# Kernel optimization log

Hardware: AMD Instinct MI355X
Metric: run time of the kernel (lower is better)

Reference implementation:

```python
import jax, jax.numpy as jnp
import numpy as np

B, FDIM = 8192, 2048
S = 10000          # number of sign nodes
D = 100            # num diseases
E = 500000         # number of 'finding' edges
ETA = 0.01


def setup_inputs() -> dict:
    key = jax.random.key(0)
    k1, k2, k3, k4, k5 = jax.random.split(key, 5)
    grad_output_batch = jax.random.normal(k1, (B, FDIM), dtype=jnp.float32)
    # similarity of each sign node per sample (0 => sign not found)
    sims = jax.random.uniform(k2, (B, S), dtype=jnp.float32)
    edge_weight = jax.random.uniform(k3, (E,), dtype=jnp.float32)
    edge_src = jax.random.randint(k4, (E,), 0, D)   # disease node per edge
    edge_dst = jax.random.randint(k5, (E,), 0, S)   # sign node per edge
    return {
        "grad_output_batch": grad_output_batch,
        "sims": sims,
        "edge_weight": edge_weight,
        "edge_src": edge_src,
        "edge_dst": edge_dst,
        "num_diseases": D,
    }


def reference(grad_output_batch, sims, edge_weight, edge_src, edge_dst, num_diseases):
    # Scatter-add edge weights into disease x sign matrix A[d, s]
    A = jnp.zeros((num_diseases, sims.shape[1]), dtype=sims.dtype)
    A = A.at[edge_src, edge_dst].add(edge_weight)
    # Per-sample gradient norm g_i = ||grad_output_batch[i]||_2
    g = jnp.linalg.norm(grad_output_batch, axis=1)            # [B]
    # nudges[i, d] = eta * g_i * sum_s sims[i, s] * A[d, s]
    nudges = ETA * g[:, None] * jnp.einsum('bs,ds->bd', sims, A)
    return nudges
```

## Files before the change

### kernel.cpp

```cpp
#include <hip/hip_runtime.h>
#include <hip/hip_bf16.h>

#define B_DIM   8192
#define FDIM    2048
#define S_DIM   10000
#define D_DIM   100
#define E_NUM   500000
#define ETA     0.01f

#define DPAD    112
#define NT      7
#define KSTEPS  313
#define KBLK    1252

typedef float  f32x4  __attribute__((ext_vector_type(4)));
typedef short  s16x8  __attribute__((ext_vector_type(8)));
typedef __bf16 bf16x8 __attribute__((ext_vector_type(8)));

__device__ inline unsigned short f2bf_bits(float x) {
    unsigned int u = __float_as_uint(x);
    unsigned int r = u + 0x7FFFu + ((u >> 16) & 1u);
    return (unsigned short)(r >> 16);
}

__global__ void scatter_kernel(const float* __restrict__ ew,
                               const int* __restrict__ esrc,
                               const int* __restrict__ edst,
                               float* __restrict__ A) {
    int e = blockIdx.x * 256 + threadIdx.x;
    if (e < E_NUM) {
        atomicAdd(&A[(size_t)esrc[e] * S_DIM + edst[e]], ew[e]);
    }
}

__global__ void build_asw_kernel(const float* __restrict__ A,
                                 unsigned short* __restrict__ Asw) {
    int t = blockIdx.x * 256 + threadIdx.x;
    int kb  = t / 896;
    int rem = t - kb * 896;
    int d   = rem >> 3;
    int s   = kb * 8 + (rem & 7);
    float v = (d < D_DIM && s < S_DIM) ? A[d * S_DIM + s] : 0.f;
    Asw[t] = f2bf_bits(v);
}

__global__ void norm_kernel(const float* __restrict__ go, float* __restrict__ g) {
    int wave = threadIdx.x >> 6;
    int lane = threadIdx.x & 63;
    int row  = blockIdx.x * 4 + wave;
    const f32x4* p = (const f32x4*)(go + (size_t)row * FDIM);
    float s = 0.f;
#pragma unroll
    for (int j = 0; j < 8; ++j) {
        f32x4 v = __builtin_nontemporal_load(p + lane + 64 * j);
        s += v[0]*v[0] + v[1]*v[1] + v[2]*v[2] + v[3]*v[3];
    }
#pragma unroll
    for (int off = 32; off; off >>= 1) s += __shfl_xor(s, off);
    if (lane == 0) g[row] = sqrtf(s);
}

__device__ inline s16x8 cvt_a(f32x4 f0, f32x4 f1) {
    bf16x8 abf;
    abf[0] = (__bf16)f0[0]; abf[1] = (__bf16)f0[1];
    abf[2] = (__bf16)f0[2]; abf[3] = (__bf16)f0[3];
    abf[4] = (__bf16)f1[0]; abf[5] = (__bf16)f1[1];
    abf[6] = (__bf16)f1[2]; abf[7] = (__bf16)f1[3];
    return __builtin_bit_cast(s16x8, abf);
}

__global__ __launch_bounds__(512, 4)
void gemm_kernel(const float* __restrict__ sims,
                 const unsigned short* __restrict__ Asw,
                 const float* __restrict__ g,
                 float* __restrict__ out) {
    __shared__ float red[8][64][29];
    const int tid  = threadIdx.x;
    const int wave = tid >> 6;
    const int lane = tid & 63;
    const int lhi  = lane >> 4;
    const int llo  = lane & 15;
    const int i0   = blockIdx.x * 16;

    const float* srow = sims + (size_t)(i0 + llo) * S_DIM + 8 * lhi;

    f32x4 acc[NT];
#pragma unroll
    for (int n = 0; n < NT; ++n) acc[n] = 0.f;

    int t = wave;
    f32x4 f0, f1;
    {
        const f32x4* p = (const f32x4*)(srow + t * 32);
        f0 = p[0]; f1 = p[1];
    }
    for (; t < 312; t += 8) {
        f32x4 n0, n1;
        n0 = 0.f; n1 = 0.f;
        const int tn = t + 8;
        if (tn < 312) {
            const f32x4* p = (const f32x4*)(srow + tn * 32);
            n0 = p[0]; n1 = p[1];
        }

        const unsigned short* bbase = Asw + ((size_t)(4 * t + lhi) * DPAD + llo) * 8;
        s16x8 b0 = *(const s16x8*)(bbase);
        s16x8 b1 = *(const s16x8*)(bbase + 128);
        s16x8 b2 = *(const s16x8*)(bbase + 256);
        s16x8 b3 = *(const s16x8*)(bbase + 384);
        s16x8 b4 = *(const s16x8*)(bbase + 512);
        s16x8 b5 = *(const s16x8*)(bbase + 640);
        s16x8 b6 = *(const s16x8*)(bbase + 768);

        s16x8 a = cvt_a(f0, f1);
        acc[0] = __builtin_amdgcn_mfma_f32_16x16x32_bf16(a, b0, acc[0], 0, 0, 0);
        acc[1] = __builtin_amdgcn_mfma_f32_16x16x32_bf16(a, b1, acc[1], 0, 0, 0);
        acc[2] = __builtin_amdgcn_mfma_f32_16x16x32_bf16(a, b2, acc[2], 0, 0, 0);
        acc[3] = __builtin_amdgcn_mfma_f32_16x16x32_bf16(a, b3, acc[3], 0, 0, 0);
        acc[4] = __builtin_amdgcn_mfma_f32_16x16x32_bf16(a, b4, acc[4], 0, 0, 0);
        acc[5] = __builtin_amdgcn_mfma_f32_16x16x32_bf16(a, b5, acc[5], 0, 0, 0);
        acc[6] = __builtin_amdgcn_mfma_f32_16x16x32_bf16(a, b6, acc[6], 0, 0, 0);

        f0 = n0; f1 = n1;
    }

    if (wave == 0) {
        f32x4 t0, t1;
        t0 = 0.f; t1 = 0.f;
        if (lhi < 2) {
            const f32x4* p = (const f32x4*)(srow + 312 * 32);
            t0 = p[0]; t1 = p[1];
        }
        const unsigned short* bbase = Asw + ((size_t)(4 * 312 + lhi) * DPAD + llo) * 8;
        s16x8 a = cvt_a(t0, t1);
#pragma unroll
        for (int n = 0; n < NT; ++n) {
            s16x8 b = *(const s16x8*)(bbase + n * 128);
            acc[n] = __builtin_amdgcn_mfma_f32_16x16x32_bf16(a, b, acc[n], 0, 0, 0);
        }
    }

#pragma unroll
    for (int n = 0; n < NT; ++n)
#pragma unroll
        for (int r = 0; r < 4; ++r)
            red[wave][lane][n * 4 + r] = acc[n][r];
    __syncthreads();

    if (wave == 0) {
        float gi[4];
#pragma unroll
        for (int r = 0; r < 4; ++r)
            gi[r] = ETA * g[i0 + lhi * 4 + r];
#pragma unroll
        for (int n = 0; n < NT; ++n) {
            int col = n * 16 + llo;
#pragma unroll
            for (int r = 0; r < 4; ++r) {
                float v = 0.f;
#pragma unroll
                for (int w = 0; w < 8; ++w) v += red[w][lane][n * 4 + r];
                if (col < D_DIM) {
                    int row = i0 + lhi * 4 + r;
                    out[row * D_DIM + col] = gi[r] * v;
                }
            }
        }
    }
}

extern "C" void kernel_launch(void* const* d_in, const int* in_sizes, int n_in,
                              void* d_out, int out_size, void* d_ws, size_t ws_size,
                              hipStream_t stream) {
    const float* grad = (const float*)d_in[0];
    const float* sims = (const float*)d_in[1];
    const float* ew   = (const float*)d_in[2];
    const int*   esrc = (const int*)d_in[3];
    const int*   edst = (const int*)d_in[4];
    float* out = (float*)d_out;

    char* ws = (char*)d_ws;
    float*          A   = (float*)ws;
    unsigned short* Asw = (unsigned short*)(ws + 4000000);
    float*          g   = (float*)(ws + 4000000 + 2243584);

    hipMemsetAsync(A, 0, (size_t)D_DIM * S_DIM * sizeof(float), stream);

    scatter_kernel  <<<(E_NUM + 255) / 256, 256, 0, stream>>>(ew, esrc, edst, A);
    build_asw_kernel<<<(KBLK * DPAD * 8) / 256, 256, 0, stream>>>(A, Asw);
    norm_kernel     <<<B_DIM / 4, 256, 0, stream>>>(grad, g);
    gemm_kernel     <<<B_DIM / 16, 512, 0, stream>>>(sims, Asw, g, out);
}
```

Measured before the change: 551.8 us.

## Restructure GEMM to split-K with LDS-shared B tiles and separate reduce

The GEMM is reorganized so each block covers 128 rows and one of 8 K-slices. Each B tile (Asw) is staged once per step into double-buffered LDS and shared by all 8 waves, instead of every wave loading B from global memory for its own K steps over 16 rows. Partial results go to a workspace slab per K-slice, and a new reduce kernel sums them and applies the eta*g scaling. This trades B-operand reuse for extra partial-sum traffic (8 slabs of B*D floats), an additional launch, and a __syncthreads each K step.

```diff
diff --git a/kernel.cpp b/kernel.cpp
--- a/kernel.cpp
+++ b/kernel.cpp
@@ -11,6 +11,8 @@
 #define DPAD    112
 #define NT      7
 #define KSTEPS  313
+#define KSPLIT  8
+#define MROWS   128
 #define KBLK    1252
 
 typedef float  f32x4  __attribute__((ext_vector_type(4)));
@@ -72,45 +74,64 @@
 __global__ __launch_bounds__(512, 4)
 void gemm_kernel(const float* __restrict__ sims,
                  const unsigned short* __restrict__ Asw,
-                 const float* __restrict__ g,
-                 float* __restrict__ out) {
-    __shared__ float red[8][64][29];
+                 float* __restrict__ part) {
+    __shared__ unsigned short buf[2][3584];
     const int tid  = threadIdx.x;
     const int wave = tid >> 6;
     const int lane = tid & 63;
     const int lhi  = lane >> 4;
     const int llo  = lane & 15;
-    const int i0   = blockIdx.x * 16;
 
-    const float* srow = sims + (size_t)(i0 + llo) * S_DIM + 8 * lhi;
+    const int kb = blockIdx.x & 7;
+    const int rb = blockIdx.x >> 3;
+    const int t0 = (KSTEPS * kb) >> 3;
+    const int t1 = (KSTEPS * (kb + 1)) >> 3;
+    const int nsteps = t1 - t0;
+
+    const int row0 = rb * MROWS + wave * 16;
+    const float* srow = sims + (size_t)(row0 + llo) * S_DIM + 8 * lhi;
 
     f32x4 acc[NT];
 #pragma unroll
     for (int n = 0; n < NT; ++n) acc[n] = 0.f;
 
-    int t = wave;
+    if (tid < 448) {
+        s16x8 v = *(const s16x8*)(Asw + (size_t)t0 * 3584 + tid * 8);
+        *(s16x8*)&buf[0][tid * 8] = v;
+    }
     f32x4 f0, f1;
     {
-        const f32x4* p = (const f32x4*)(srow + t * 32);
+        const f32x4* p = (const f32x4*)(srow + t0 * 32);
         f0 = p[0]; f1 = p[1];
     }
-    for (; t < 312; t += 8) {
-        f32x4 n0, n1;
-        n0 = 0.f; n1 = 0.f;
-        const int tn = t + 8;
-        if (tn < 312) {
-            const f32x4* p = (const f32x4*)(srow + tn * 32);
-            n0 = p[0]; n1 = p[1];
+    __syncthreads();
+
+    for (int i = 0; i < nsteps; ++i) {
+        const int t = t0 + i;
+        const int cur = i & 1;
+
+        if (i + 1 < nsteps && tid < 448) {
+            s16x8 v = *(const s16x8*)(Asw + (size_t)(t + 1) * 3584 + tid * 8);
+            *(s16x8*)&buf[cur ^ 1][tid * 8] = v;
         }
 
-        const unsigned short* bbase = Asw + ((size_t)(4 * t + lhi) * DPAD + llo) * 8;
-        s16x8 b0 = *(const s16x8*)(bbase);
-        s16x8 b1 = *(const s16x8*)(bbase + 128);
-        s16x8 b2 = *(const s16x8*)(bbase + 256);
-        s16x8 b3 = *(const s16x8*)(bbase + 384);
-        s16x8 b4 = *(const s16x8*)(bbase + 512);
-        s16x8 b5 = *(const s16x8*)(bbase + 640);
-        s16x8 b6 = *(const s16x8*)(bbase + 768);
+        f32x4 n0 = 0.f, n1 = 0.f;
+        {
+            const int kn = (t + 1) * 32 + 8 * lhi;
+            if (i + 1 < nsteps && kn <= S_DIM - 8) {
+                const f32x4* p = (const f32x4*)(srow + (size_t)(t + 1) * 32);
+                n0 = p[0]; n1 = p[1];
+            }
+        }
+
+        const unsigned short* bb = &buf[cur][lhi * 896 + llo * 8];
+        s16x8 b0 = *(const s16x8*)(bb);
+        s16x8 b1 = *(const s16x8*)(bb + 128);
+        s16x8 b2 = *(const s16x8*)(bb + 256);
+        s16x8 b3 = *(const s16x8*)(bb + 384);
+        s16x8 b4 = *(const s16x8*)(bb + 512);
+        s16x8 b5 = *(const s16x8*)(bb + 640);
+        s16x8 b6 = *(const s16x8*)(bb + 768);
 
         s16x8 a = cvt_a(f0, f1);
         acc[0] = __builtin_amdgcn_mfma_f32_16x16x32_bf16(a, b0, acc[0], 0, 0, 0);
@@ -122,50 +143,33 @@
         acc[6] = __builtin_amdgcn_mfma_f32_16x16x32_bf16(a, b6, acc[6], 0, 0, 0);
 
         f0 = n0; f1 = n1;
+        __syncthreads();
     }
 
-    if (wave == 0) {
-        f32x4 t0, t1;
-        t0 = 0.f; t1 = 0.f;
-        if (lhi < 2) {
-            const f32x4* p = (const f32x4*)(srow + 312 * 32);
-            t0 = p[0]; t1 = p[1];
-        }
-        const unsigned short* bbase = Asw + ((size_t)(4 * 312 + lhi) * DPAD + llo) * 8;
-        s16x8 a = cvt_a(t0, t1);
+    float* pslab = part + (size_t)kb * (B_DIM * D_DIM);
+    const int rbase = row0 + lhi * 4;
 #pragma unroll
-        for (int n = 0; n < NT; ++n) {
-            s16x8 b = *(const s16x8*)(bbase + n * 128);
-            acc[n] = __builtin_amdgcn_mfma_f32_16x16x32_bf16(a, b, acc[n], 0, 0, 0);
+    for (int n = 0; n < NT; ++n) {
+        const int col = n * 16 + llo;
+        if (col < D_DIM) {
+#pragma unroll
+            for (int r = 0; r < 4; ++r)
+                pslab[(size_t)(rbase + r) * D_DIM + col] = acc[n][r];
         }
     }
+}
 
+__global__ void reduce_kernel(const float* __restrict__ part,
+                              const float* __restrict__ g,
+                              float* __restrict__ out) {
+    int idx = blockIdx.x * 256 + threadIdx.x;
+    if (idx < B_DIM * D_DIM) {
+        float s = 0.f;
 #pragma unroll
-    for (int n = 0; n < NT; ++n)
-#pragma unroll
-        for (int r = 0; r < 4; ++r)
-            red[wave][lane][n * 4 + r] = acc[n][r];
-    __syncthreads();
-
-    if (wave == 0) {
-        float gi[4];
-#pragma unroll
-        for (int r = 0; r < 4; ++r)
-            gi[r] = ETA * g[i0 + lhi * 4 + r];
-#pragma unroll
-        for (int n = 0; n < NT; ++n) {
-            int col = n * 16 + llo;
-#pragma unroll
-            for (int r = 0; r < 4; ++r) {
-                float v = 0.f;
-#pragma unroll
-                for (int w = 0; w < 8; ++w) v += red[w][lane][n * 4 + r];
-                if (col < D_DIM) {
-                    int row = i0 + lhi * 4 + r;
-                    out[row * D_DIM + col] = gi[r] * v;
-                }
-            }
-        }
+        for (int kb = 0; kb < KSPLIT; ++kb)
+            s += part[(size_t)kb * (B_DIM * D_DIM) + idx];
+        int i = idx / D_DIM;
+        out[idx] = ETA * g[i] * s;
     }
 }
 
@@ -180,14 +184,16 @@
     float* out = (float*)d_out;
 
     char* ws = (char*)d_ws;
-    float*          A   = (float*)ws;
-    unsigned short* Asw = (unsigned short*)(ws + 4000000);
-    float*          g   = (float*)(ws + 4000000 + 2243584);
+    float*          A    = (float*)(ws);
+    unsigned short* Asw  = (unsigned short*)(ws + (4 << 20));
+    float*          g    = (float*)(ws + (7 << 20));
+    float*          part = (float*)(ws + (8 << 20));
 
     hipMemsetAsync(A, 0, (size_t)D_DIM * S_DIM * sizeof(float), stream);
 
     scatter_kernel  <<<(E_NUM + 255) / 256, 256, 0, stream>>>(ew, esrc, edst, A);
     build_asw_kernel<<<(KBLK * DPAD * 8) / 256, 256, 0, stream>>>(A, Asw);
     norm_kernel     <<<B_DIM / 4, 256, 0, stream>>>(grad, g);
-    gemm_kernel     <<<B_DIM / 16, 512, 0, stream>>>(sims, Asw, g, out);
+    gemm_kernel     <<<64 * KSPLIT, 512, 0, stream>>>(sims, Asw, part);
+    reduce_kernel   <<<(B_DIM * D_DIM + 255) / 256, 256, 0, stream>>>(part, g, out);
 }
```

New measurement: 517.2 us. -6.3%, faster.
